# Optimization experiments

Measured on AMD Instinct MI355X. Metric: run time of the kernel, lower is better.

The kernel has to match this reference:

```python
import jax, jax.numpy as jnp
import numpy as np

N, E, G = 65536, 524288, 1024
ND, ED, HID, H, C = 21, 12, 128, 4, 32
L = 8  # num_blocks * 2 conv layers
EPS = 1e-5


def _gatv2(x, src, dst, ea, Wl, Wr, We, att, bias):
    # PyG GATv2Conv: xl=lin_l(x) (source), xr=lin_r(x) (target)
    n = x.shape[0]
    xl = jnp.einsum('nd,dhc->nhc', x, Wl)   # [N,H,C]
    xr = jnp.einsum('nd,dhc->nhc', x, Wr)
    el = jnp.einsum('ed,dhc->ehc', ea, We)  # [E,H,C]
    m = xl[src] + xr[dst] + el              # per-edge message pre-activation
    e = jnp.einsum('ehc,hc->eh', jax.nn.leaky_relu(m, 0.2), att)  # [E,H]
    # scatter softmax over incoming edges of each dst node
    emax = jax.ops.segment_max(e, dst, num_segments=n)
    emax = jnp.where(jnp.isfinite(emax), emax, 0.0)
    p = jnp.exp(e - emax[dst])
    denom = jax.ops.segment_sum(p, dst, num_segments=n)
    alpha = p / jnp.clip(denom, 1e-16)[dst]
    out = jax.ops.segment_sum(alpha[..., None] * xl[src], dst, num_segments=n)
    return out.reshape(n, H * C) + bias


def _bn(x, scale, bias):
    mu = x.mean(0)
    var = x.var(0)
    return (x - mu) * jax.lax.rsqrt(var + EPS) * scale + bias


def setup_inputs():
    key = jax.random.key(0)
    ks = jax.random.split(key, 16)
    f = lambda k, shp, s=0.05: jax.random.normal(k, shp, jnp.float32) * s
    return dict(
        x=f(ks[0], (N, ND), 1.0),
        edge_attr=f(ks[1], (E, ED), 1.0),
        edge_index=jax.random.randint(ks[2], (2, E), 0, N),
        batch=jnp.sort(jax.random.randint(ks[3], (N,), 0, G)),
        Win=f(ks[4], (ND, HID)), bin_=jnp.zeros(HID),
        Wl=f(ks[5], (L, HID, H, C)), Wr=f(ks[6], (L, HID, H, C)),
        We=f(ks[7], (L, ED, H, C)), att=f(ks[8], (L, H, C)),
        bconv=jnp.zeros((L, HID)),
        bn_scale=jnp.ones((L, HID)), bn_bias=jnp.zeros((L, HID)),
        Wv1=f(ks[9], (HID, 64)), bv1=jnp.zeros(64),
        Wv2=f(ks[10], (64, 3)), bv2=jnp.zeros(3),
        Wp1=f(ks[11], (2 * HID + ED, 64)), bp1=jnp.zeros(64),
        Wp2=f(ks[12], (64, 1)), bp2=jnp.zeros(1),
    )


def reference(x, edge_attr, edge_index, batch, Win, bin_, Wl, Wr, We, att,
              bconv, bn_scale, bn_bias, Wv1, bv1, Wv2, bv2, Wp1, bp1, Wp2, bp2):
    src0, dst0 = edge_index[0], edge_index[1]
    # add_self_loops with fill_value='mean' for edge features
    ones_e = jnp.ones((E,), x.dtype)
    deg = jax.ops.segment_sum(ones_e, dst0, num_segments=N)
    mean_ea = jax.ops.segment_sum(edge_attr, dst0, num_segments=N) / jnp.clip(deg, 1.0)[:, None]
    ar = jnp.arange(N)
    src = jnp.concatenate([src0, ar])
    dst = jnp.concatenate([dst0, ar])
    ea = jnp.concatenate([edge_attr, mean_ea], axis=0)

    h = jax.nn.relu(x @ Win + bin_)
    for b in range(L // 2):
        i, j = 2 * b, 2 * b + 1
        res = h
        h = _gatv2(h, src, dst, ea, Wl[i], Wr[i], We[i], att[i], bconv[i])
        h = jax.nn.relu(_bn(h, bn_scale[i], bn_bias[i]))
        h = _gatv2(h, src, dst, ea, Wl[j], Wr[j], We[j], att[j], bconv[j])
        h = _bn(h, bn_scale[j], bn_bias[j])
        h = jax.nn.relu(h + res)

    counts = jax.ops.segment_sum(jnp.ones((N,), h.dtype), batch, num_segments=G)
    pooled = jax.ops.segment_sum(h, batch, num_segments=G) / jnp.clip(counts, 1.0)[:, None]
    value_logits = jax.nn.relu(pooled @ Wv1 + bv1) @ Wv2 + bv2  # [G,3]

    edge_input = jnp.concatenate([h[src0], h[dst0], edge_attr], axis=1)  # [E, 2*HID+ED]
    policy_logits = (jax.nn.relu(edge_input @ Wp1 + bp1) @ Wp2 + bp2)[:, 0]  # [E]
    return value_logits, policy_logits
```

## Files before the change

kernel.cpp:

```cpp
#include <hip/hip_runtime.h>

#define NN 65536
#define EE 524288
#define EPX 589824
#define GG 1024
#define NSLOT 16

typedef __attribute__((ext_vector_type(8))) short bf16x8;
typedef __attribute__((ext_vector_type(4))) float f32x4;


__device__ __forceinline__ unsigned short f2bf(float x) {
    unsigned int u = __float_as_uint(x);
    u += 0x7FFFu + ((u >> 16) & 1u);
    return (unsigned short)(u >> 16);
}
__device__ __forceinline__ float bflo(unsigned int w) { return __uint_as_float(w << 16); }
__device__ __forceinline__ float bfhi(unsigned int w) { return __uint_as_float(w & 0xFFFF0000u); }
__device__ __forceinline__ float lrelu(float x) { return fmaf(0.4f, fabsf(x), 0.6f * x); }


__launch_bounds__(256)
__global__ void k_deg(const int* __restrict__ dst0, int* __restrict__ deg)
{
    int e = blockIdx.x * 256 + threadIdx.x;
    if (e >= EE) return;
    atomicAdd(&deg[dst0[e]], 1);
}

__launch_bounds__(1024)
__global__ void k_scan(const int* __restrict__ deg, int* __restrict__ rowptr)
{
    __shared__ int sums[1024];
    int t = threadIdx.x;
    int base = t * 64;
    int s = 0;
    for (int i = 0; i < 64; i++) s += deg[base + i] + 1;
    sums[t] = s;
    __syncthreads();
    for (int off = 1; off < 1024; off <<= 1) {
        int v = (t >= off) ? sums[t - off] : 0;
        __syncthreads();
        sums[t] += v;
        __syncthreads();
    }
    int off = sums[t] - s;
    for (int i = 0; i < 64; i++) { rowptr[base + i] = off; off += deg[base + i] + 1; }
    if (t == 1023) rowptr[NN] = off;
}

__launch_bounds__(256)
__global__ void k_scatter(const int* __restrict__ src0, const int* __restrict__ dst0,
                          const float* __restrict__ eattr,
                          const int* __restrict__ rowptr, const int* __restrict__ deg,
                          int* __restrict__ fill, int* __restrict__ csr_src,
                          unsigned short* __restrict__ eaCSR)
{
    int e = blockIdx.x * 256 + threadIdx.x;
    if (e >= EPX) return;
    if (e < EE) {
        int d = dst0[e];
        int pos = rowptr[d] + atomicAdd(&fill[d], 1);
        csr_src[pos] = src0[e];
        const float* ep = eattr + (size_t)e * 12;
        float4 a = *reinterpret_cast<const float4*>(ep);
        float4 b = *reinterpret_cast<const float4*>(ep + 4);
        float4 c = *reinterpret_cast<const float4*>(ep + 8);
        unsigned int w0 = (unsigned int)f2bf(a.x) | ((unsigned int)f2bf(a.y) << 16);
        unsigned int w1 = (unsigned int)f2bf(a.z) | ((unsigned int)f2bf(a.w) << 16);
        unsigned int w2 = (unsigned int)f2bf(b.x) | ((unsigned int)f2bf(b.y) << 16);
        unsigned int w3 = (unsigned int)f2bf(b.z) | ((unsigned int)f2bf(b.w) << 16);
        unsigned int w4 = (unsigned int)f2bf(c.x) | ((unsigned int)f2bf(c.y) << 16);
        unsigned int w5 = (unsigned int)f2bf(c.z) | ((unsigned int)f2bf(c.w) << 16);
        uint2* q = reinterpret_cast<uint2*>(eaCSR + (size_t)pos * 12);
        q[0] = make_uint2(w0, w1);
        q[1] = make_uint2(w2, w3);
        q[2] = make_uint2(w4, w5);
    } else {
        int n = e - EE;
        csr_src[rowptr[n] + deg[n]] = n;
    }
}

__launch_bounds__(256)
__global__ void k_selfattr(const int* __restrict__ rowptr, unsigned short* __restrict__ eaCSR)
{
    int tid = blockIdx.x * 256 + threadIdx.x;
    int n = tid >> 4;
    int lk = tid & 15;
    if (lk >= 12) return;
    int beg = rowptr[n], endm1 = rowptr[n + 1] - 1;
    float s = 0.f;
    for (int p = beg; p < endm1; ++p)
        s += __uint_as_float(((unsigned int)eaCSR[(size_t)p * 12 + lk]) << 16);
    float dv = fmaxf((float)(endm1 - beg), 1.0f);
    eaCSR[(size_t)endm1 * 12 + lk] = f2bf(s / dv);
}


__launch_bounds__(256)
__global__ void k_wprep(const float* __restrict__ Wl, const float* __restrict__ Wr,
                        const float* __restrict__ Wp1,
                        unsigned short* __restrict__ wg, unsigned short* __restrict__ wp)
{
    int tid = blockIdx.x * 256 + threadIdx.x;
    if (tid < 32768) {
        int l = tid >> 12;
        int r = tid & 4095;
        int kt = r >> 10, ct = (r >> 6) & 15, lane = r & 63;
        int kb = kt * 32 + (lane >> 4) * 8;
        int col = ct * 16 + (lane & 15);
        const float* W = (col < 128) ? (Wl + (size_t)l * 16384 + col)
                                     : (Wr + (size_t)l * 16384 + (col - 128));
        unsigned short* o = wg + (size_t)tid * 8;
#pragma unroll
        for (int j = 0; j < 8; j++) o[j] = f2bf(W[(size_t)(kb + j) * 128]);
    } else if (tid < 34816) {
        int r = tid - 32768;
        int kt = r >> 9, ct = (r >> 6) & 7, lane = r & 63;
        int kb = kt * 32 + (lane >> 4) * 8;
        int col = ct * 16 + (lane & 15);
        const float* W = (col < 64) ? (Wp1 + col) : (Wp1 + 128 * 64 + (col - 64));
        unsigned short* o = wp + (size_t)r * 8;
#pragma unroll
        for (int j = 0; j < 8; j++) o[j] = f2bf(W[(size_t)(kb + j) * 64]);
    }
}


__launch_bounds__(256)
__global__ void k_input(const float* __restrict__ x, const float* __restrict__ Win,
                        const float* __restrict__ bin, float* __restrict__ h)
{
    __shared__ float W[21 * 128];
    int t = threadIdx.x;
    for (int i = t; i < 21 * 128; i += 256) W[i] = Win[i];
    __syncthreads();
    int c = t & 127, sub = t >> 7;
    int n0 = blockIdx.x * 16;
    float bc = bin[c];
    for (int i = 0; i < 8; i++) {
        int n = n0 + sub + i * 2;
        const float* xp = x + (size_t)n * 21;
        float acc = bc;
#pragma unroll
        for (int k = 0; k < 21; k++) acc = fmaf(xp[k], W[k * 128 + c], acc);
        h[(size_t)n * 128 + c] = fmaxf(acc, 0.f);
    }
}


__device__ __forceinline__ void load_afrag(const float* __restrict__ A, int arow, int kb,
                                           bf16x8 af[4])
{
#pragma unroll
    for (int kt = 0; kt < 4; kt++) {
        const float* ap = A + (size_t)arow * 128 + kt * 32 + kb;
        float4 lo = *reinterpret_cast<const float4*>(ap);
        float4 hi = *reinterpret_cast<const float4*>(ap + 4);
        bf16x8 v;
        v[0] = (short)f2bf(lo.x); v[1] = (short)f2bf(lo.y);
        v[2] = (short)f2bf(lo.z); v[3] = (short)f2bf(lo.w);
        v[4] = (short)f2bf(hi.x); v[5] = (short)f2bf(hi.y);
        v[6] = (short)f2bf(hi.z); v[7] = (short)f2bf(hi.w);
        af[kt] = v;
    }
}

__device__ __forceinline__ void gemm_gat_core(const bf16x8 af[4], const unsigned short* __restrict__ Bf,
                                              int row0, unsigned short* __restrict__ Cl,
                                              unsigned short* __restrict__ Cr, int lane)
{
    int crow = row0 + (lane >> 4) * 4;
    int c0 = lane & 15;
#pragma unroll
    for (int ct = 0; ct < 16; ct++) {
        f32x4 acc = {0.f, 0.f, 0.f, 0.f};
#pragma unroll
        for (int kt = 0; kt < 4; kt++) {
            bf16x8 bf = *reinterpret_cast<const bf16x8*>(Bf + ((size_t)(kt * 16 + ct) * 64 + lane) * 8);
            acc = __builtin_amdgcn_mfma_f32_16x16x32_bf16(af[kt], bf, acc, 0, 0, 0);
        }
        int col = ct * 16 + c0;
        unsigned short* C = (col < 128) ? Cl : Cr;
        int cc = col & 127;
#pragma unroll
        for (int r = 0; r < 4; r++)
            C[(size_t)(crow + r) * 128 + cc] = f2bf(acc[r]);
    }
}

__launch_bounds__(256)
__global__ void k_gemm_gat(const float* __restrict__ A, const unsigned short* __restrict__ Bf,
                           unsigned short* __restrict__ Cl, unsigned short* __restrict__ Cr)
{
    int wave = threadIdx.x >> 6, lane = threadIdx.x & 63;
    int row0 = blockIdx.x * 64 + wave * 16;
    bf16x8 af[4];
    load_afrag(A, row0 + (lane & 15), (lane >> 4) * 8, af);
    gemm_gat_core(af, Bf, row0, Cl, Cr, lane);
}

__launch_bounds__(256)
__global__ void k_gemm_gat_bn(const float* __restrict__ G, const float* __restrict__ bnstat,
                              const float* __restrict__ scale, const float* __restrict__ bias,
                              const unsigned short* __restrict__ Bf,
                              unsigned short* __restrict__ Cl, unsigned short* __restrict__ Cr)
{
    __shared__ float sA[128], bA[128];
    int t = threadIdx.x;
    if (t < 128) {
        float sum = 0.f, sq = 0.f;
#pragma unroll
        for (int sl = 0; sl < NSLOT; sl++) {
            sum += bnstat[sl * 256 + t];
            sq  += bnstat[sl * 256 + 128 + t];
        }
        const float invN = 1.0f / (float)NN;
        float mean = sum * invN;
        float var  = sq * invN - mean * mean;
        float sc   = scale[t] * rsqrtf(var + 1e-5f);
        sA[t] = sc;
        bA[t] = bias[t] - mean * sc;
    }
    __syncthreads();
    int wave = t >> 6, lane = t & 63;
    int row0 = blockIdx.x * 64 + wave * 16;
    int arow = row0 + (lane & 15);
    int kb = (lane >> 4) * 8;
    bf16x8 af[4];
#pragma unroll
    for (int kt = 0; kt < 4; kt++) {
        int cb = kt * 32 + kb;
        const float* gp = G + (size_t)arow * 128 + cb;
        float4 lo = *reinterpret_cast<const float4*>(gp);
        float4 hi = *reinterpret_cast<const float4*>(gp + 4);
        bf16x8 v;
        v[0] = (short)f2bf(fmaxf(fmaf(lo.x, sA[cb + 0], bA[cb + 0]), 0.f));
        v[1] = (short)f2bf(fmaxf(fmaf(lo.y, sA[cb + 1], bA[cb + 1]), 0.f));
        v[2] = (short)f2bf(fmaxf(fmaf(lo.z, sA[cb + 2], bA[cb + 2]), 0.f));
        v[3] = (short)f2bf(fmaxf(fmaf(lo.w, sA[cb + 3], bA[cb + 3]), 0.f));
        v[4] = (short)f2bf(fmaxf(fmaf(hi.x, sA[cb + 4], bA[cb + 4]), 0.f));
        v[5] = (short)f2bf(fmaxf(fmaf(hi.y, sA[cb + 5], bA[cb + 5]), 0.f));
        v[6] = (short)f2bf(fmaxf(fmaf(hi.z, sA[cb + 6], bA[cb + 6]), 0.f));
        v[7] = (short)f2bf(fmaxf(fmaf(hi.w, sA[cb + 7], bA[cb + 7]), 0.f));
        af[kt] = v;
    }
    gemm_gat_core(af, Bf, row0, Cl, Cr, lane);
}

__launch_bounds__(256)
__global__ void k_gemm_pol(const float* __restrict__ A, const unsigned short* __restrict__ Bf,
                           float* __restrict__ P)
{
    int wave = threadIdx.x >> 6, lane = threadIdx.x & 63;
    int row0 = blockIdx.x * 64 + wave * 16;
    bf16x8 af[4];
    load_afrag(A, row0 + (lane & 15), (lane >> 4) * 8, af);
    int crow = row0 + (lane >> 4) * 4;
    int c0 = lane & 15;
#pragma unroll
    for (int ct = 0; ct < 8; ct++) {
        f32x4 acc = {0.f, 0.f, 0.f, 0.f};
#pragma unroll
        for (int kt = 0; kt < 4; kt++) {
            bf16x8 bf = *reinterpret_cast<const bf16x8*>(Bf + ((size_t)(kt * 8 + ct) * 64 + lane) * 8);
            acc = __builtin_amdgcn_mfma_f32_16x16x32_bf16(af[kt], bf, acc, 0, 0, 0);
        }
        int col = ct * 16 + c0;
#pragma unroll
        for (int r = 0; r < 4; r++)
            P[(size_t)(crow + r) * 128 + col] = acc[r];
    }
}


__launch_bounds__(256)
__global__ void k_gat(const unsigned short* __restrict__ xlb, const unsigned short* __restrict__ xrb,
                      const unsigned short* __restrict__ eaCSR,
                      const int* __restrict__ rowptr, const int* __restrict__ csr_src,
                      const float* __restrict__ We, const float* __restrict__ att,
                      const float* __restrict__ bconv, float* __restrict__ g,
                      float* __restrict__ bnstat)
{
    int wid = blockIdx.x * 4 + (threadIdx.x >> 6);
    int lane = threadIdx.x & 63;
    int f0 = lane * 2;

    float2 wxy[12];
#pragma unroll
    for (int k = 0; k < 12; k++)
        wxy[k] = *reinterpret_cast<const float2*>(We + k * 128 + f0);
    float2 av = *reinterpret_cast<const float2*>(att + f0);
    float2 bc = *reinterpret_cast<const float2*>(bconv + f0);

    float bs0 = 0.f, bs1 = 0.f, bq0 = 0.f, bq1 = 0.f;

    for (int n = wid * 8; n < wid * 8 + 8; ++n) {
        unsigned int xrw = *reinterpret_cast<const unsigned int*>(xrb + (size_t)n * 128 + f0);
        float xr0 = bflo(xrw), xr1 = bfhi(xrw);

        float m = -INFINITY, s = 0.f, a0 = 0.f, a1 = 0.f;
        int beg = rowptr[n], end = rowptr[n + 1];
        int idx = beg;
        for (; idx + 2 <= end; idx += 2) {
            int s0 = csr_src[idx], s1 = csr_src[idx + 1];
            const uint2* q0 = reinterpret_cast<const uint2*>(eaCSR + (size_t)idx * 12);
            uint2 qa = q0[0], qb = q0[1], qc = q0[2];
            uint2 ra = q0[3], rb = q0[4], rc = q0[5];
            unsigned int xw0 = *reinterpret_cast<const unsigned int*>(xlb + (size_t)s0 * 128 + f0);
            unsigned int xw1 = *reinterpret_cast<const unsigned int*>(xlb + (size_t)s1 * 128 + f0);

            float e0[12], e1[12];
            e0[0] = bflo(qa.x); e0[1] = bfhi(qa.x); e0[2]  = bflo(qa.y); e0[3]  = bfhi(qa.y);
            e0[4] = bflo(qb.x); e0[5] = bfhi(qb.x); e0[6]  = bflo(qb.y); e0[7]  = bfhi(qb.y);
            e0[8] = bflo(qc.x); e0[9] = bfhi(qc.x); e0[10] = bflo(qc.y); e0[11] = bfhi(qc.y);
            e1[0] = bflo(ra.x); e1[1] = bfhi(ra.x); e1[2]  = bflo(ra.y); e1[3]  = bfhi(ra.y);
            e1[4] = bflo(rb.x); e1[5] = bfhi(rb.x); e1[6]  = bflo(rb.y); e1[7]  = bfhi(rb.y);
            e1[8] = bflo(rc.x); e1[9] = bfhi(rc.x); e1[10] = bflo(rc.y); e1[11] = bfhi(rc.y);

            float2 el0 = {0.f, 0.f}, el1 = {0.f, 0.f};
#pragma unroll
            for (int k = 0; k < 12; k++) {
                el0.x = fmaf(e0[k], wxy[k].x, el0.x); el0.y = fmaf(e0[k], wxy[k].y, el0.y);
                el1.x = fmaf(e1[k], wxy[k].x, el1.x); el1.y = fmaf(e1[k], wxy[k].y, el1.y);
            }
            float xa0 = bflo(xw0), xa1 = bfhi(xw0);
            float xb0 = bflo(xw1), xb1 = bfhi(xw1);

            float t0 = lrelu(xa0 + xr0 + el0.x) * av.x + lrelu(xa1 + xr1 + el0.y) * av.y;
            float t1 = lrelu(xb0 + xr0 + el1.x) * av.x + lrelu(xb1 + xr1 + el1.y) * av.y;
            t0 += __shfl_xor(t0, 1);  t1 += __shfl_xor(t1, 1);
            t0 += __shfl_xor(t0, 2);  t1 += __shfl_xor(t1, 2);
            t0 += __shfl_xor(t0, 4);  t1 += __shfl_xor(t1, 4);
            t0 += __shfl_xor(t0, 8);  t1 += __shfl_xor(t1, 8);

            float nm = fmaxf(m, fmaxf(t0, t1));
            float so = __expf(m - nm);
            float w0 = __expf(t0 - nm);
            float w1 = __expf(t1 - nm);
            s  = fmaf(s, so, w0 + w1);
            a0 = fmaf(a0, so, fmaf(w0, xa0, w1 * xb0));
            a1 = fmaf(a1, so, fmaf(w0, xa1, w1 * xb1));
            m = nm;
        }
        if (idx < end) {
            int s0 = csr_src[idx];
            const uint2* q0 = reinterpret_cast<const uint2*>(eaCSR + (size_t)idx * 12);
            uint2 qa = q0[0], qb = q0[1], qc = q0[2];
            unsigned int xw0 = *reinterpret_cast<const unsigned int*>(xlb + (size_t)s0 * 128 + f0);
            float e0[12];
            e0[0] = bflo(qa.x); e0[1] = bfhi(qa.x); e0[2]  = bflo(qa.y); e0[3]  = bfhi(qa.y);
            e0[4] = bflo(qb.x); e0[5] = bfhi(qb.x); e0[6]  = bflo(qb.y); e0[7]  = bfhi(qb.y);
            e0[8] = bflo(qc.x); e0[9] = bfhi(qc.x); e0[10] = bflo(qc.y); e0[11] = bfhi(qc.y);
            float2 el0 = {0.f, 0.f};
#pragma unroll
            for (int k = 0; k < 12; k++) {
                el0.x = fmaf(e0[k], wxy[k].x, el0.x); el0.y = fmaf(e0[k], wxy[k].y, el0.y);
            }
            float xa0 = bflo(xw0), xa1 = bfhi(xw0);
            float tt = lrelu(xa0 + xr0 + el0.x) * av.x + lrelu(xa1 + xr1 + el0.y) * av.y;
            tt += __shfl_xor(tt, 1);
            tt += __shfl_xor(tt, 2);
            tt += __shfl_xor(tt, 4);
            tt += __shfl_xor(tt, 8);
            float nm = fmaxf(m, tt);
            float so = __expf(m - nm);
            float w  = __expf(tt - nm);
            s  = fmaf(s, so, w);
            a0 = fmaf(a0, so, w * xa0);
            a1 = fmaf(a1, so, w * xa1);
            m = nm;
        }
        float inv = 1.f / s;
        float r0 = fmaf(a0, inv, bc.x);
        float r1 = fmaf(a1, inv, bc.y);
        *reinterpret_cast<float2*>(g + (size_t)n * 128 + f0) = make_float2(r0, r1);
        bs0 += r0; bs1 += r1;
        bq0 = fmaf(r0, r0, bq0); bq1 = fmaf(r1, r1, bq1);
    }

    __shared__ float red[256 * 4];
    int t = threadIdx.x;
    red[t * 4 + 0] = bs0; red[t * 4 + 1] = bs1;
    red[t * 4 + 2] = bq0; red[t * 4 + 3] = bq1;
    __syncthreads();
    if (t < 64) {
        float v0 = red[t * 4 + 0] + red[(t + 64) * 4 + 0] + red[(t + 128) * 4 + 0] + red[(t + 192) * 4 + 0];
        float v1 = red[t * 4 + 1] + red[(t + 64) * 4 + 1] + red[(t + 128) * 4 + 1] + red[(t + 192) * 4 + 1];
        float q0 = red[t * 4 + 2] + red[(t + 64) * 4 + 2] + red[(t + 128) * 4 + 2] + red[(t + 192) * 4 + 2];
        float q1 = red[t * 4 + 3] + red[(t + 64) * 4 + 3] + red[(t + 128) * 4 + 3] + red[(t + 192) * 4 + 3];
        float* slot = bnstat + (size_t)(blockIdx.x & (NSLOT - 1)) * 256;
        atomicAdd(&slot[2 * t + 0], v0);
        atomicAdd(&slot[2 * t + 1], v1);
        atomicAdd(&slot[128 + 2 * t + 0], q0);
        atomicAdd(&slot[128 + 2 * t + 1], q1);
    }
}


__launch_bounds__(256)
__global__ void k_bnapply_res_relu(const float4* __restrict__ gin,
                                   const float* __restrict__ bnstat,
                                   const float* __restrict__ scale, const float* __restrict__ bias,
                                   float4* __restrict__ hbuf)
{
    __shared__ float sA[128], bA[128];
    int t = threadIdx.x;
    if (t < 128) {
        float sum = 0.f, sq = 0.f;
#pragma unroll
        for (int sl = 0; sl < NSLOT; sl++) {
            sum += bnstat[sl * 256 + t];
            sq  += bnstat[sl * 256 + 128 + t];
        }
        const float invN = 1.0f / (float)NN;
        float mean = sum * invN;
        float var  = sq * invN - mean * mean;
        float sc   = scale[t] * rsqrtf(var + 1e-5f);
        sA[t] = sc;
        bA[t] = bias[t] - mean * sc;
    }
    __syncthreads();
    int idx = blockIdx.x * 256 + t;
    int c4 = (idx & 31) * 4;
    float4 v = gin[idx];
    float4 hv = hbuf[idx];
    float4 r;
    r.x = fmaxf(fmaf(v.x, sA[c4 + 0], bA[c4 + 0]) + hv.x, 0.f);
    r.y = fmaxf(fmaf(v.y, sA[c4 + 1], bA[c4 + 1]) + hv.y, 0.f);
    r.z = fmaxf(fmaf(v.z, sA[c4 + 2], bA[c4 + 2]) + hv.z, 0.f);
    r.w = fmaxf(fmaf(v.w, sA[c4 + 3], bA[c4 + 3]) + hv.w, 0.f);
    hbuf[idx] = r;
}


__launch_bounds__(128)
__global__ void k_pool(const float* __restrict__ h, const int* __restrict__ batch,
                       float* __restrict__ pooled, float* __restrict__ cnt)
{
    int c = threadIdx.x;
    int r0 = blockIdx.x * 128;
    int cur = batch[r0];
    float acc = 0.f;
    float run = 0.f;
    for (int i = 0; i < 128; ++i) {
        int r = r0 + i;
        int b = batch[r];
        if (b != cur) {
            atomicAdd(&pooled[(size_t)cur * 128 + c], acc);
            if (c == 0) atomicAdd(&cnt[cur], run);
            acc = 0.f; run = 0.f; cur = b;
        }
        acc += h[(size_t)r * 128 + c];
        run += 1.f;
    }
    atomicAdd(&pooled[(size_t)cur * 128 + c], acc);
    if (c == 0) atomicAdd(&cnt[cur], run);
}

__launch_bounds__(64)
__global__ void k_value(const float* __restrict__ pooled, const float* __restrict__ cnt,
                        const float* __restrict__ Wv1, const float* __restrict__ bv1,
                        const float* __restrict__ Wv2, const float* __restrict__ bv2,
                        float* __restrict__ out)
{
    int gi = blockIdx.x;
    int l = threadIdx.x;
    float inv = 1.f / fmaxf(cnt[gi], 1.f);
    const float* pr = pooled + (size_t)gi * 128;
    float z = bv1[l];
    for (int k = 0; k < 128; k++) z = fmaf(pr[k] * inv, Wv1[k * 64 + l], z);
    z = fmaxf(z, 0.f);
#pragma unroll
    for (int j = 0; j < 3; j++) {
        float p = z * Wv2[l * 3 + j];
        p += __shfl_xor(p, 32); p += __shfl_xor(p, 16); p += __shfl_xor(p, 8);
        p += __shfl_xor(p, 4);  p += __shfl_xor(p, 2);  p += __shfl_xor(p, 1);
        if (l == 0) out[gi * 3 + j] = p + bv2[j];
    }
}


__launch_bounds__(256)
__global__ void k_policy(const float* __restrict__ P,
                         const float* __restrict__ eattr,
                         const int* __restrict__ src0, const int* __restrict__ dst0,
                         const float* __restrict__ Wp1c, const float* __restrict__ bp1,
                         const float* __restrict__ Wp2, const float* __restrict__ bp2,
                         float* __restrict__ out)
{
    int wave = (blockIdx.x * 256 + threadIdx.x) >> 6;
    int lane = threadIdx.x & 63;
    float w1c[12];
#pragma unroll
    for (int k = 0; k < 12; k++) w1c[k] = Wp1c[k * 64 + lane];
    float wp2 = Wp2[lane];
    float bb = bp1[lane];
    float b2 = bp2[0];
    for (int i = 0; i < 8; i++) {
        int e = wave * 8 + i;
        int sI = src0[e], dI = dst0[e];
        const float* ep = eattr + (size_t)e * 12;
        float4 e0 = *reinterpret_cast<const float4*>(ep);
        float4 e1 = *reinterpret_cast<const float4*>(ep + 4);
        float4 e2 = *reinterpret_cast<const float4*>(ep + 8);
        float z = P[(size_t)sI * 128 + lane] + P[(size_t)dI * 128 + 64 + lane] + bb;
        z += e0.x * w1c[0] + e0.y * w1c[1] + e0.z * w1c[2]  + e0.w * w1c[3]
           + e1.x * w1c[4] + e1.y * w1c[5] + e1.z * w1c[6]  + e1.w * w1c[7]
           + e2.x * w1c[8] + e2.y * w1c[9] + e2.z * w1c[10] + e2.w * w1c[11];
        z = fmaxf(z, 0.f);
        float p = z * wp2;
        p += __shfl_xor(p, 32); p += __shfl_xor(p, 16); p += __shfl_xor(p, 8);
        p += __shfl_xor(p, 4);  p += __shfl_xor(p, 2);  p += __shfl_xor(p, 1);
        if (lane == 0) out[3072 + e] = p + b2;
    }
}


extern "C" void kernel_launch(void* const* d_in, const int* in_sizes, int n_in,
                              void* d_out, int out_size, void* d_ws, size_t ws_size,
                              hipStream_t stream)
{
    const float* x     = (const float*)d_in[0];
    const float* eattr = (const float*)d_in[1];
    const int*   eidx  = (const int*)d_in[2];
    const int*   batch = (const int*)d_in[3];
    const float* Win   = (const float*)d_in[4];
    const float* bin   = (const float*)d_in[5];
    const float* Wl    = (const float*)d_in[6];
    const float* Wr    = (const float*)d_in[7];
    const float* We    = (const float*)d_in[8];
    const float* att   = (const float*)d_in[9];
    const float* bconv = (const float*)d_in[10];
    const float* bnsc  = (const float*)d_in[11];
    const float* bnbi  = (const float*)d_in[12];
    const float* Wv1   = (const float*)d_in[13];
    const float* bv1   = (const float*)d_in[14];
    const float* Wv2   = (const float*)d_in[15];
    const float* bv2   = (const float*)d_in[16];
    const float* Wp1   = (const float*)d_in[17];
    const float* bp1   = (const float*)d_in[18];
    const float* Wp2   = (const float*)d_in[19];
    const float* bp2   = (const float*)d_in[20];
    float* out = (float*)d_out;

    const int* src0 = eidx;
    const int* dst0 = eidx + EE;

    const size_t NH = (size_t)NN * 128;
    float* ws = (float*)d_ws;
    float* h  = ws;
    float* g  = h + NH;
    unsigned short* xlb = (unsigned short*)(g + NH);
    unsigned short* xrb = xlb + NH;
    unsigned short* eaCSR = xrb + NH;
    int* rowptr = (int*)(eaCSR + (size_t)EPX * 12);
    int* csr_src = rowptr + (NN + 1);
    int* deg  = csr_src + EPX;
    int* fill = deg + NN;
    float* bnstat = (float*)(fill + NN);
    float* pooled = bnstat + 8 * NSLOT * 256;
    float* cnt    = pooled + (size_t)GG * 128;
    size_t zero_elems = (size_t)NN + NN + 8 * NSLOT * 256 + (size_t)GG * 128 + GG;
    unsigned short* wg = (unsigned short*)(cnt + GG);
    unsigned short* wp = wg + 8 * 32768;

    hipMemsetAsync(deg, 0, zero_elems * sizeof(float), stream);

    k_deg<<<EE / 256, 256, 0, stream>>>(dst0, deg);
    k_scan<<<1, 1024, 0, stream>>>(deg, rowptr);
    k_scatter<<<EPX / 256, 256, 0, stream>>>(src0, dst0, eattr, rowptr, deg, fill, csr_src, eaCSR);
    k_selfattr<<<(NN * 16) / 256, 256, 0, stream>>>(rowptr, eaCSR);
    k_wprep<<<136, 256, 0, stream>>>(Wl, Wr, Wp1, wg, wp);

    k_input<<<NN / 16, 256, 0, stream>>>(x, Win, bin, h);

    for (int l = 0; l < 8; l++) {
        float* bs = bnstat + (size_t)l * NSLOT * 256;
        if (l % 2 == 0) {
            k_gemm_gat<<<NN / 64, 256, 0, stream>>>(h, wg + (size_t)l * 32768, xlb, xrb);
        } else {
            float* bsp = bnstat + (size_t)(l - 1) * NSLOT * 256;
            k_gemm_gat_bn<<<NN / 64, 256, 0, stream>>>(g, bsp,
                                                       bnsc + (size_t)(l - 1) * 128,
                                                       bnbi + (size_t)(l - 1) * 128,
                                                       wg + (size_t)l * 32768, xlb, xrb);
        }
        k_gat<<<NN / 32, 256, 0, stream>>>(xlb, xrb, eaCSR, rowptr, csr_src,
                                           We + (size_t)l * 1536, att + (size_t)l * 128,
                                           bconv + (size_t)l * 128, g, bs);
        if (l % 2 == 1) {
            k_bnapply_res_relu<<<(NN * 128 / 4) / 256, 256, 0, stream>>>(
                (const float4*)g, bs, bnsc + (size_t)l * 128, bnbi + (size_t)l * 128,
                (float4*)h);
        }
    }

    k_pool<<<NN / 128, 128, 0, stream>>>(h, batch, pooled, cnt);
    k_value<<<GG, 64, 0, stream>>>(pooled, cnt, Wv1, bv1, Wv2, bv2, out);

    float* P = g;
    k_gemm_pol<<<NN / 64, 256, 0, stream>>>(h, wp, P);
    k_policy<<<NN / 4, 256, 0, stream>>>(P, eattr, src0, dst0,
                                         Wp1 + 256 * 64, bp1, Wp2, bp2, out);
}
```

Baseline: 1.269 ms.

## Use packed fp16 edge features and half2 FMA for edge projection in GAT

Stores edge attributes as fp16 instead of bf16 so the per-edge 12-dim projection can use packed half2 FMAs instead of unpacking to 24 scalar fp32 FMAs. Also pre-shifts CSR source indices into byte offsets to drop address arithmetic in the gather, and folds log2(e) into the attention vector so exp2f replaces __expf. This cuts ALU work in the GAT edge loop at the cost of fp16 accumulation precision for the edge projection and the fp16 range limits. Any other consumer of csr_src (e.g. the policy head, if it reads it) would now see shifted indices.

```diff
diff --git a/kernel.cpp b/kernel.cpp
--- a/kernel.cpp
+++ b/kernel.cpp
@@ -1,4 +1,5 @@
 #include <hip/hip_runtime.h>
+#include <hip/hip_fp16.h>
 
 #define NN 65536
 #define EE 524288
@@ -9,6 +10,8 @@
 typedef __attribute__((ext_vector_type(8))) short bf16x8;
 typedef __attribute__((ext_vector_type(4))) float f32x4;
 
+#define LOG2E 1.44269504088896f
+
 
 __device__ __forceinline__ unsigned short f2bf(float x) {
     unsigned int u = __float_as_uint(x);
@@ -18,6 +21,10 @@
 __device__ __forceinline__ float bflo(unsigned int w) { return __uint_as_float(w << 16); }
 __device__ __forceinline__ float bfhi(unsigned int w) { return __uint_as_float(w & 0xFFFF0000u); }
 __device__ __forceinline__ float lrelu(float x) { return fmaf(0.4f, fabsf(x), 0.6f * x); }
+__device__ __forceinline__ unsigned int packh2(float a, float b) {
+    __half2 h = __floats2half2_rn(a, b);
+    return *reinterpret_cast<unsigned int*>(&h);
+}
 
 
 __launch_bounds__(256)
@@ -61,24 +68,18 @@
     if (e < EE) {
         int d = dst0[e];
         int pos = rowptr[d] + atomicAdd(&fill[d], 1);
-        csr_src[pos] = src0[e];
+        csr_src[pos] = src0[e] << 8;
         const float* ep = eattr + (size_t)e * 12;
         float4 a = *reinterpret_cast<const float4*>(ep);
         float4 b = *reinterpret_cast<const float4*>(ep + 4);
         float4 c = *reinterpret_cast<const float4*>(ep + 8);
-        unsigned int w0 = (unsigned int)f2bf(a.x) | ((unsigned int)f2bf(a.y) << 16);
-        unsigned int w1 = (unsigned int)f2bf(a.z) | ((unsigned int)f2bf(a.w) << 16);
-        unsigned int w2 = (unsigned int)f2bf(b.x) | ((unsigned int)f2bf(b.y) << 16);
-        unsigned int w3 = (unsigned int)f2bf(b.z) | ((unsigned int)f2bf(b.w) << 16);
-        unsigned int w4 = (unsigned int)f2bf(c.x) | ((unsigned int)f2bf(c.y) << 16);
-        unsigned int w5 = (unsigned int)f2bf(c.z) | ((unsigned int)f2bf(c.w) << 16);
         uint2* q = reinterpret_cast<uint2*>(eaCSR + (size_t)pos * 12);
-        q[0] = make_uint2(w0, w1);
-        q[1] = make_uint2(w2, w3);
-        q[2] = make_uint2(w4, w5);
+        q[0] = make_uint2(packh2(a.x, a.y), packh2(a.z, a.w));
+        q[1] = make_uint2(packh2(b.x, b.y), packh2(b.z, b.w));
+        q[2] = make_uint2(packh2(c.x, c.y), packh2(c.z, c.w));
     } else {
         int n = e - EE;
-        csr_src[rowptr[n] + deg[n]] = n;
+        csr_src[rowptr[n] + deg[n]] = n << 8;
     }
 }
 
@@ -91,10 +92,13 @@
     if (lk >= 12) return;
     int beg = rowptr[n], endm1 = rowptr[n + 1] - 1;
     float s = 0.f;
-    for (int p = beg; p < endm1; ++p)
-        s += __uint_as_float(((unsigned int)eaCSR[(size_t)p * 12 + lk]) << 16);
+    for (int p = beg; p < endm1; ++p) {
+        __half h = *reinterpret_cast<const __half*>(&eaCSR[(size_t)p * 12 + lk]);
+        s += __half2float(h);
+    }
     float dv = fmaxf((float)(endm1 - beg), 1.0f);
-    eaCSR[(size_t)endm1 * 12 + lk] = f2bf(s / dv);
+    __half ho = __float2half(s / dv);
+    eaCSR[(size_t)endm1 * 12 + lk] = *reinterpret_cast<unsigned short*>(&ho);
 }
 
 
@@ -275,6 +279,29 @@
 }
 
 
+__device__ __forceinline__ float2 edge_el(uint2 qa, uint2 qb, uint2 qc,
+                                          const __half2 wx[6], const __half2 wy[6])
+{
+    __half2 e0 = *reinterpret_cast<const __half2*>(&qa.x);
+    __half2 e1 = *reinterpret_cast<const __half2*>(&qa.y);
+    __half2 e2 = *reinterpret_cast<const __half2*>(&qb.x);
+    __half2 e3 = *reinterpret_cast<const __half2*>(&qb.y);
+    __half2 e4 = *reinterpret_cast<const __half2*>(&qc.x);
+    __half2 e5 = *reinterpret_cast<const __half2*>(&qc.y);
+    __half2 ax = __hmul2(e0, wx[0]);
+    ax = __hfma2(e1, wx[1], ax); ax = __hfma2(e2, wx[2], ax);
+    ax = __hfma2(e3, wx[3], ax); ax = __hfma2(e4, wx[4], ax);
+    ax = __hfma2(e5, wx[5], ax);
+    __half2 ay = __hmul2(e0, wy[0]);
+    ay = __hfma2(e1, wy[1], ay); ay = __hfma2(e2, wy[2], ay);
+    ay = __hfma2(e3, wy[3], ay); ay = __hfma2(e4, wy[4], ay);
+    ay = __hfma2(e5, wy[5], ay);
+    float2 r;
+    r.x = __low2float(ax) + __high2float(ax);
+    r.y = __low2float(ay) + __high2float(ay);
+    return r;
+}
+
 __launch_bounds__(256)
 __global__ void k_gat(const unsigned short* __restrict__ xlb, const unsigned short* __restrict__ xrb,
                       const unsigned short* __restrict__ eaCSR,
@@ -287,12 +314,18 @@
     int lane = threadIdx.x & 63;
     int f0 = lane * 2;
 
-    float2 wxy[12];
-#pragma unroll
-    for (int k = 0; k < 12; k++)
-        wxy[k] = *reinterpret_cast<const float2*>(We + k * 128 + f0);
+    __half2 wx[6], wy[6];
+#pragma unroll
+    for (int j = 0; j < 6; j++) {
+        float2 w0 = *reinterpret_cast<const float2*>(We + (2 * j) * 128 + f0);
+        float2 w1 = *reinterpret_cast<const float2*>(We + (2 * j + 1) * 128 + f0);
+        wx[j] = __floats2half2_rn(w0.x, w1.x);
+        wy[j] = __floats2half2_rn(w0.y, w1.y);
+    }
     float2 av = *reinterpret_cast<const float2*>(att + f0);
+    av.x *= LOG2E; av.y *= LOG2E;
     float2 bc = *reinterpret_cast<const float2*>(bconv + f0);
+    const char* xl_lane = reinterpret_cast<const char*>(xlb) + (lane << 2);
 
     float bs0 = 0.f, bs1 = 0.f, bq0 = 0.f, bq1 = 0.f;
 
@@ -304,27 +337,16 @@
         int beg = rowptr[n], end = rowptr[n + 1];
         int idx = beg;
         for (; idx + 2 <= end; idx += 2) {
-            int s0 = csr_src[idx], s1 = csr_src[idx + 1];
+            int off0 = csr_src[idx], off1 = csr_src[idx + 1];
             const uint2* q0 = reinterpret_cast<const uint2*>(eaCSR + (size_t)idx * 12);
             uint2 qa = q0[0], qb = q0[1], qc = q0[2];
             uint2 ra = q0[3], rb = q0[4], rc = q0[5];
-            unsigned int xw0 = *reinterpret_cast<const unsigned int*>(xlb + (size_t)s0 * 128 + f0);
-            unsigned int xw1 = *reinterpret_cast<const unsigned int*>(xlb + (size_t)s1 * 128 + f0);
-
-            float e0[12], e1[12];
-            e0[0] = bflo(qa.x); e0[1] = bfhi(qa.x); e0[2]  = bflo(qa.y); e0[3]  = bfhi(qa.y);
-            e0[4] = bflo(qb.x); e0[5] = bfhi(qb.x); e0[6]  = bflo(qb.y); e0[7]  = bfhi(qb.y);
-            e0[8] = bflo(qc.x); e0[9] = bfhi(qc.x); e0[10] = bflo(qc.y); e0[11] = bfhi(qc.y);
-            e1[0] = bflo(ra.x); e1[1] = bfhi(ra.x); e1[2]  = bflo(ra.y); e1[3]  = bfhi(ra.y);
-            e1[4] = bflo(rb.x); e1[5] = bfhi(rb.x); e1[6]  = bflo(rb.y); e1[7]  = bfhi(rb.y);
-            e1[8] = bflo(rc.x); e1[9] = bfhi(rc.x); e1[10] = bflo(rc.y); e1[11] = bfhi(rc.y);
-
-            float2 el0 = {0.f, 0.f}, el1 = {0.f, 0.f};
-#pragma unroll
-            for (int k = 0; k < 12; k++) {
-                el0.x = fmaf(e0[k], wxy[k].x, el0.x); el0.y = fmaf(e0[k], wxy[k].y, el0.y);
-                el1.x = fmaf(e1[k], wxy[k].x, el1.x); el1.y = fmaf(e1[k], wxy[k].y, el1.y);
-            }
+            unsigned int xw0 = *reinterpret_cast<const unsigned int*>(xl_lane + off0);
+            unsigned int xw1 = *reinterpret_cast<const unsigned int*>(xl_lane + off1);
+
+            float2 el0 = edge_el(qa, qb, qc, wx, wy);
+            float2 el1 = edge_el(ra, rb, rc, wx, wy);
+
             float xa0 = bflo(xw0), xa1 = bfhi(xw0);
             float xb0 = bflo(xw1), xb1 = bfhi(xw1);
 
@@ -336,28 +358,20 @@
             t0 += __shfl_xor(t0, 8);  t1 += __shfl_xor(t1, 8);
 
             float nm = fmaxf(m, fmaxf(t0, t1));
-            float so = __expf(m - nm);
-            float w0 = __expf(t0 - nm);
-            float w1 = __expf(t1 - nm);
+            float so = exp2f(m - nm);
+            float w0 = exp2f(t0 - nm);
+            float w1 = exp2f(t1 - nm);
             s  = fmaf(s, so, w0 + w1);
             a0 = fmaf(a0, so, fmaf(w0, xa0, w1 * xb0));
             a1 = fmaf(a1, so, fmaf(w0, xa1, w1 * xb1));
             m = nm;
         }
         if (idx < end) {
-            int s0 = csr_src[idx];
+            int off0 = csr_src[idx];
             const uint2* q0 = reinterpret_cast<const uint2*>(eaCSR + (size_t)idx * 12);
             uint2 qa = q0[0], qb = q0[1], qc = q0[2];
-            unsigned int xw0 = *reinterpret_cast<const unsigned int*>(xlb + (size_t)s0 * 128 + f0);
-            float e0[12];
-            e0[0] = bflo(qa.x); e0[1] = bfhi(qa.x); e0[2]  = bflo(qa.y); e0[3]  = bfhi(qa.y);
-            e0[4] = bflo(qb.x); e0[5] = bfhi(qb.x); e0[6]  = bflo(qb.y); e0[7]  = bfhi(qb.y);
-            e0[8] = bflo(qc.x); e0[9] = bfhi(qc.x); e0[10] = bflo(qc.y); e0[11] = bfhi(qc.y);
-            float2 el0 = {0.f, 0.f};
-#pragma unroll
-            for (int k = 0; k < 12; k++) {
-                el0.x = fmaf(e0[k], wxy[k].x, el0.x); el0.y = fmaf(e0[k], wxy[k].y, el0.y);
-            }
+            unsigned int xw0 = *reinterpret_cast<const unsigned int*>(xl_lane + off0);
+            float2 el0 = edge_el(qa, qb, qc, wx, wy);
             float xa0 = bflo(xw0), xa1 = bfhi(xw0);
             float tt = lrelu(xa0 + xr0 + el0.x) * av.x + lrelu(xa1 + xr1 + el0.y) * av.y;
             tt += __shfl_xor(tt, 1);
@@ -365,8 +379,8 @@
             tt += __shfl_xor(tt, 4);
             tt += __shfl_xor(tt, 8);
             float nm = fmaxf(m, tt);
-            float so = __expf(m - nm);
-            float w  = __expf(tt - nm);
+            float so = exp2f(m - nm);
+            float w  = exp2f(tt - nm);
             s  = fmaf(s, so, w);
             a0 = fmaf(a0, so, w * xa0);
             a1 = fmaf(a1, so, w * xa1);
```

Measured after the change: 1.202 ms. -5.3%, faster.
